# Kernel tuning notes

Hardware: AMD Instinct MI355X
Metric: run time of the kernel (lower is better)

Reference implementation:

```python
import jax, jax.numpy as jnp
import numpy as np

WINDOW = 1024  # sliding-window mask_mod: attend to keys within WINDOW behind the query


def setup_inputs() -> dict:
    key = jax.random.key(0)
    B, L, H, E = 2, 2048, 16, 64
    qkv = jax.random.normal(key, (B, L, 3, H, E), dtype=jnp.float32)
    return {"qkv": qkv}


def reference(qkv) -> jnp.ndarray:
    # Training path of FlexAttention.forward (key_cache/val_cache/cache_seqlens = None).
    B, L, _, H, E = qkv.shape
    q = qkv[:, :, 0]  # [b, l, h, e]
    k = qkv[:, :, 1]
    v = qkv[:, :, 2]

    scale = 1.0 / (E ** 0.5)  # flex_attention default softmax scaling
    scores = jnp.einsum("bqhe,bkhe->bhqk", q, k) * scale  # [b, h, q, kv]

    q_idx = jnp.arange(L)[:, None]
    kv_idx = jnp.arange(L)[None, :]
    dist = q_idx - kv_idx  # [q, kv]

    # score_mod: ALiBi bias, slope_h = 2^(-8*(h+1)/H)
    slopes = jnp.exp2(-8.0 * (jnp.arange(H, dtype=jnp.float32) + 1.0) / H)
    scores = scores - slopes[None, :, None, None] * dist.astype(jnp.float32)

    # and_masks(mask_mod, causal_mask): sliding window AND causal
    mask = (dist >= 0) & (dist < WINDOW)  # causal guarantees >=1 valid key per row
    scores = jnp.where(mask[None, None], scores, -jnp.inf)

    attn = jax.nn.softmax(scores, axis=-1)
    out = jnp.einsum("bhqk,bkhe->bqhe", attn, v)  # [b, l, h, e]
    return out
```

## Files before the change

kernel.cpp:

```cpp
#include <hip/hip_runtime.h>
#include <cstdint>

#define L_SEQ 2048
#define NH 16
#define EDIM 64
#define WINDOW 1024
#define QT 64
#define KT 64
#define LOG2E 1.4426950408889634f
#define M_FIX 16.0f

typedef short bf16x8 __attribute__((ext_vector_type(8)));
typedef short bf16x4 __attribute__((ext_vector_type(4)));
typedef float f32x4 __attribute__((ext_vector_type(4)));

__device__ __forceinline__ short f2bf(float x) {
    uint32_t u = __builtin_bit_cast(uint32_t, x);
    uint32_t r = (u + 0x7fffu + ((u >> 16) & 1u)) >> 16;
    return (short)(r & 0xffffu);
}
__device__ __forceinline__ short f2bf_trunc(float x) {
    return (short)(__builtin_bit_cast(uint32_t, x) >> 16);
}

__device__ __forceinline__ f32x4 mfma16(bf16x4 a, bf16x4 b, f32x4 c) {
#if __has_builtin(__builtin_amdgcn_mfma_f32_16x16x16bf16_1k)
    return __builtin_amdgcn_mfma_f32_16x16x16bf16_1k(a, b, c, 0, 0, 0);
#else
    asm("s_nop 1\n\tv_mfma_f32_16x16x16_bf16 %0, %1, %2, %0"
        : "+v"(c) : "v"(a), "v"(b));
    return c;
#endif
}

__device__ __forceinline__ void async16(const short* g, const short* l) {
    __builtin_amdgcn_global_load_lds(
        (const __attribute__((address_space(1))) void*)(uintptr_t)(g),
        (__attribute__((address_space(3))) void*)(uintptr_t)(l),
        16, 0, 0);
}

__global__ __launch_bounds__(256) void prepass4(const float* __restrict__ qkv,
        short* __restrict__ kw, short* __restrict__ vw) {
    __shared__ float vt[64][68];
    const int x = blockIdx.x;
    const int xcd = x & 7, y = x >> 3;
    const int pairid = xcd * 4 + (y >> 5);
    const int tile = y & 31;
    const int b = pairid >> 4, h = pairid & 15;
    const int tid = threadIdx.x;
    const int tg = pairid * 32 + tile;
    const float* base = qkv + (size_t)b * (L_SEQ * 3072) + (size_t)tile * 64 * 3072 + h * 64;
    short* ko = kw + (size_t)tg * 4096;
    short* vo = vw + (size_t)tg * 4096;

    #pragma unroll
    for (int it = 0; it < 2; ++it) {
        const int c = tid + it * 256;
        const int row = c >> 3, cc = (c & 7) ^ (row & 7);
        const float* src = base + (size_t)row * 3072 + 1024 + cc * 8;
        float4 a = *(const float4*)src, d = *(const float4*)(src + 4);
        short* o = ko + (size_t)c * 8;
        o[0] = f2bf(a.x); o[1] = f2bf(a.y); o[2] = f2bf(a.z); o[3] = f2bf(a.w);
        o[4] = f2bf(d.x); o[5] = f2bf(d.y); o[6] = f2bf(d.z); o[7] = f2bf(d.w);
    }
    {
        const int row = tid >> 2, e0 = (tid & 3) << 4;
        const float* src = base + (size_t)row * 3072 + 2048 + e0;
        #pragma unroll
        for (int q4 = 0; q4 < 4; ++q4) {
            float4 a = *(const float4*)(src + q4 * 4);
            vt[e0 + q4 * 4 + 0][row] = a.x;
            vt[e0 + q4 * 4 + 1][row] = a.y;
            vt[e0 + q4 * 4 + 2][row] = a.z;
            vt[e0 + q4 * 4 + 3][row] = a.w;
        }
    }
    __syncthreads();
    #pragma unroll
    for (int it = 0; it < 2; ++it) {
        const int c = tid + it * 256;
        const int et = c >> 7, a = (c >> 6) & 1, l6 = c & 63;
        const int quad = l6 >> 4, r16 = l6 & 15;
        const int e = et * 16 + r16;
        float4 x0 = *(const float4*)&vt[e][a * 32 + quad * 4];
        float4 x1 = *(const float4*)&vt[e][a * 32 + 16 + quad * 4];
        bf16x8 o8;
        o8[0] = f2bf(x0.x); o8[1] = f2bf(x0.y); o8[2] = f2bf(x0.z); o8[3] = f2bf(x0.w);
        o8[4] = f2bf(x1.x); o8[5] = f2bf(x1.y); o8[6] = f2bf(x1.z); o8[7] = f2bf(x1.w);
        *(bf16x8*)(vo + (size_t)c * 8) = o8;
    }
}

__global__ __launch_bounds__(256, 4) void flexattn_fwd7(
        const float* __restrict__ qkv, const short* __restrict__ kw,
        const short* __restrict__ vw, float* __restrict__ out) {
    __shared__ __align__(16) short kS[2][4096];
    __shared__ __align__(16) short vS[2][4096];

    const int s = blockIdx.y & 31;
    const int k = blockIdx.y >> 5;
    const int t16 = (s + ((k >> 1) << 4)) & 31;
    const int qtile = (k & 1) ? (31 - t16) : t16;
    const int pairid = blockIdx.x * 4 + k;
    const int h = pairid & 15;
    const int b = pairid >> 4;

    const int tid   = threadIdx.x;
    const int w     = tid >> 6;
    const int lane  = tid & 63;
    const int quad  = lane >> 4;
    const int r16   = lane & 15;
    const int qhalf = w & 1;
    const int khalf = w >> 1;
    const int qb    = qtile * QT;
    const int bh32  = (b * NH + h) * 32;
    const int q0    = qb + qhalf * 32 + r16;

    const int t0q = (qb >= WINDOW - 1) ? ((qb - (WINDOW - 1)) >> 6) : 0;
    const int t1  = qtile;
    const int swz = quad ^ (r16 & 7);
    const int cb0 = w * 128;

    {
        const short* ktile = kw + (size_t)(bh32 + t0q) * 4096;
        const short* vtile = vw + (size_t)(bh32 + t0q) * 4096;
        #pragma unroll
        for (int i = 0; i < 2; ++i) {
            const int cb = cb0 + i * 64;
            async16(ktile + (size_t)(cb + lane) * 8, &kS[0][cb * 8]);
            async16(vtile + (size_t)(cb + lane) * 8, &vS[0][cb * 8]);
        }
    }

    const float qscale = 0.125f * LOG2E;
    bf16x8 qfrag[2][2];
    #pragma unroll
    for (int g = 0; g < 2; ++g) {
        const float* qrow = qkv + (size_t)b * (L_SEQ * 3072)
                                + (size_t)(q0 + g * 16) * 3072 + h * 64;
        #pragma unroll
        for (int es = 0; es < 2; ++es) {
            const float* p = qrow + es * 32 + quad * 8;
            float4 a = *(const float4*)p;
            float4 c = *(const float4*)(p + 4);
            bf16x8 f;
            f[0] = f2bf(a.x * qscale); f[1] = f2bf(a.y * qscale);
            f[2] = f2bf(a.z * qscale); f[3] = f2bf(a.w * qscale);
            f[4] = f2bf(c.x * qscale); f[5] = f2bf(c.y * qscale);
            f[6] = f2bf(c.z * qscale); f[7] = f2bf(c.w * qscale);
            qfrag[g][es] = f;
        }
    }

    const float slope2 = __builtin_amdgcn_exp2f(-8.0f * (float)(h + 1) / (float)NH) * LOG2E;
    const float c64 = slope2 * 64.0f;
    f32x4 EA[2][2];
    #pragma unroll
    for (int g = 0; g < 2; ++g)
        #pragma unroll
        for (int ctl = 0; ctl < 2; ++ctl)
            #pragma unroll
            for (int r = 0; r < 4; ++r)
                EA[g][ctl][r] = slope2 * (float)(t0q * 64 + (khalf * 2 + ctl) * 16
                                                 + quad * 4 + r - (q0 + g * 16)) - M_FIX;

    f32x4 O[2][4] = {};
    float rs[2] = {0.f, 0.f};

    for (int kt = t0q; kt <= t1; ++kt) {
        const int cur = (kt - t0q) & 1;
        __syncthreads();
        if (kt < t1) {
            const int nb = cur ^ 1;
            const short* ktile = kw + (size_t)(bh32 + kt + 1) * 4096;
            const short* vtile = vw + (size_t)(bh32 + kt + 1) * 4096;
            #pragma unroll
            for (int i = 0; i < 2; ++i) {
                const int cb = cb0 + i * 64;
                async16(ktile + (size_t)(cb + lane) * 8, &kS[nb][cb * 8]);
                async16(vtile + (size_t)(cb + lane) * 8, &vS[nb][cb * 8]);
            }
        }

        f32x4 S[2][2];
        __builtin_amdgcn_s_setprio(1);
        #pragma unroll
        for (int ctl = 0; ctl < 2; ++ctl) {
            const int ct = khalf * 2 + ctl;
            const int c0 = ((ct * 16 + r16) << 3) + swz;
            bf16x8 k0 = *(const bf16x8*)&kS[cur][c0 * 8];
            bf16x8 k1 = *(const bf16x8*)&kS[cur][(c0 ^ 4) * 8];
            #pragma unroll
            for (int g = 0; g < 2; ++g) {
                f32x4 acc = __builtin_amdgcn_mfma_f32_16x16x32_bf16(k0, qfrag[g][0], EA[g][ctl], 0, 0, 0);
                S[g][ctl] = __builtin_amdgcn_mfma_f32_16x16x32_bf16(k1, qfrag[g][1], acc, 0, 0, 0);
            }
        }
        __builtin_amdgcn_s_setprio(0);

        bf16x4 pb[2][2];
        if (kt != t0q && kt != t1) {
            #pragma unroll
            for (int g = 0; g < 2; ++g)
                #pragma unroll
                for (int ctl = 0; ctl < 2; ++ctl)
                    #pragma unroll
                    for (int r = 0; r < 4; ++r) {
                        const float pe = __builtin_amdgcn_exp2f(S[g][ctl][r]);
                        rs[g] += pe;
                        pb[g][ctl][r] = f2bf_trunc(pe);
                    }
        } else {
            const int key0 = kt * 64 + khalf * 32 + quad * 4;
            #pragma unroll
            for (int g = 0; g < 2; ++g) {
                const int qg = q0 + g * 16;
                #pragma unroll
                for (int ctl = 0; ctl < 2; ++ctl)
                    #pragma unroll
                    for (int r = 0; r < 4; ++r) {
                        const int dist = qg - (key0 + ctl * 16 + r);
                        float pe = __builtin_amdgcn_exp2f(S[g][ctl][r]);
                        pe = (dist < 0 || dist >= WINDOW) ? 0.0f : pe;
                        rs[g] += pe;
                        pb[g][ctl][r] = f2bf_trunc(pe);
                    }
            }
        }

        __builtin_amdgcn_s_setprio(1);
        #pragma unroll
        for (int et = 0; et < 4; ++et) {
            bf16x8 v8 = *(const bf16x8*)&vS[cur][(size_t)((et * 2 + khalf) * 64 + lane) * 8];
            bf16x4 vlo = {v8[0], v8[1], v8[2], v8[3]};
            bf16x4 vhi = {v8[4], v8[5], v8[6], v8[7]};
            #pragma unroll
            for (int g = 0; g < 2; ++g) {
                O[g][et] = mfma16(vlo, pb[g][0], O[g][et]);
                O[g][et] = mfma16(vhi, pb[g][1], O[g][et]);
            }
        }
        __builtin_amdgcn_s_setprio(0);

        #pragma unroll
        for (int ctl = 0; ctl < 2; ++ctl) {
            EA[0][ctl] += c64;
            EA[1][ctl] += c64;
        }
    }

    __syncthreads();
    float* oS = (float*)&kS[0][0];
    float* rS = (float*)&vS[0][0];
    if (khalf) {
        float* dst = oS + qhalf * 2048;
        #pragma unroll
        for (int g = 0; g < 2; ++g)
            #pragma unroll
            for (int et = 0; et < 4; ++et)
                #pragma unroll
                for (int j = 0; j < 4; ++j)
                    dst[((g * 4 + et) * 4 + j) * 64 + lane] = O[g][et][j];
        rS[qhalf * 128 + lane]      = rs[0];
        rS[qhalf * 128 + 64 + lane] = rs[1];
    }
    __syncthreads();
    if (!khalf) {
        const float* src = oS + qhalf * 2048;
        #pragma unroll
        for (int g = 0; g < 2; ++g)
            #pragma unroll
            for (int et = 0; et < 4; ++et)
                #pragma unroll
                for (int j = 0; j < 4; ++j)
                    O[g][et][j] += src[((g * 4 + et) * 4 + j) * 64 + lane];
        rs[0] += rS[qhalf * 128 + lane];
        rs[1] += rS[qhalf * 128 + 64 + lane];

        #pragma unroll
        for (int g = 0; g < 2; ++g) {
            float r = rs[g];
            r += __shfl_xor(r, 16, 64);
            r += __shfl_xor(r, 32, 64);
            const float rl = 1.0f / r;
            float* op = out + ((size_t)b * L_SEQ + (q0 + g * 16)) * (NH * EDIM) + h * EDIM;
            #pragma unroll
            for (int et = 0; et < 4; ++et) {
                float4 o4 = {O[g][et][0] * rl, O[g][et][1] * rl,
                             O[g][et][2] * rl, O[g][et][3] * rl};
                *(float4*)(op + et * 16 + quad * 4) = o4;
            }
        }
    }
}

__global__ __launch_bounds__(256, 2) void flexattn_fwd_fb(
        const float* __restrict__ qkv, float* __restrict__ out) {
    __shared__ __align__(16) short kT[KT * 72];
    __shared__ __align__(16) short vB[8 * 64 * 8];
    __shared__ __align__(16) short pT[4][16 * 72];

    const int qtile = blockIdx.x;
    const int h     = blockIdx.y;
    const int b     = blockIdx.z;
    const int tid   = threadIdx.x;
    const int w     = tid >> 6;
    const int lane  = tid & 63;
    const int quad  = lane >> 4;
    const int r16   = lane & 15;
    const int qb = qtile * QT;
    const int rowstride = 3 * NH * EDIM;

    const float* qbase = qkv + ((size_t)b * L_SEQ * 3 + 0) * (NH * EDIM) + h * EDIM;
    const float* kbase = qkv + ((size_t)b * L_SEQ * 3 + 1) * (NH * EDIM) + h * EDIM;
    const float* vbase = qkv + ((size_t)b * L_SEQ * 3 + 2) * (NH * EDIM) + h * EDIM;

    const float qscale = 0.125f * LOG2E;
    bf16x8 qfrag[2];
    {
        const int qg = qb + w * 16 + r16;
        const float* qrow = qbase + (size_t)qg * rowstride;
        #pragma unroll
        for (int es = 0; es < 2; ++es) {
            const float* p = qrow + es * 32 + quad * 8;
            float4 a = *(const float4*)p;
            float4 c = *(const float4*)(p + 4);
            bf16x8 f;
            f[0] = f2bf(a.x * qscale); f[1] = f2bf(a.y * qscale);
            f[2] = f2bf(a.z * qscale); f[3] = f2bf(a.w * qscale);
            f[4] = f2bf(c.x * qscale); f[5] = f2bf(c.y * qscale);
            f[6] = f2bf(c.z * qscale); f[7] = f2bf(c.w * qscale);
            qfrag[es] = f;
        }
    }

    const float slope2 = __builtin_amdgcn_exp2f(-8.0f * (float)(h + 1) / (float)NH) * LOG2E;
    f32x4 O[4] = {{0,0,0,0},{0,0,0,0},{0,0,0,0},{0,0,0,0}};
    float m_run[4] = {-1e30f, -1e30f, -1e30f, -1e30f};
    float l_run[4] = {0.f, 0.f, 0.f, 0.f};

    const int kmin = (qb >= WINDOW - 1) ? (qb - (WINDOW - 1)) : 0;
    const int t0 = kmin >> 6;
    const int t1 = qtile;

    for (int kt = t0; kt <= t1; ++kt) {
        __syncthreads();
        {
            const int j = tid >> 2;
            const int ebase = (tid & 3) * 16;
            const float* krow = kbase + (size_t)(kt * KT + j) * rowstride + ebase;
            const float* vrow = vbase + (size_t)(kt * KT + j) * rowstride + ebase;
            const int js = j >> 5, qd = (j >> 3) & 3, ii = j & 7;
            #pragma unroll
            for (int ee = 0; ee < 4; ++ee) {
                const int e = ebase + ee * 4;
                float4 k4 = *(const float4*)(krow + ee * 4);
                short* kd = &kT[j * 72 + e];
                kd[0] = f2bf(k4.x); kd[1] = f2bf(k4.y);
                kd[2] = f2bf(k4.z); kd[3] = f2bf(k4.w);
                float4 v4 = *(const float4*)(vrow + ee * 4);
                const int et = e >> 4;
                const int ln = qd * 16 + (e & 15);
                short* vd = &vB[(((js * 4 + et) * 64) + ln) * 8 + ii];
                vd[0]  = f2bf(v4.x);
                vd[8]  = f2bf(v4.y);
                vd[16] = f2bf(v4.z);
                vd[24] = f2bf(v4.w);
            }
        }
        __syncthreads();

        f32x4 S[4];
        #pragma unroll
        for (int ct = 0; ct < 4; ++ct) {
            const short* kr = &kT[(ct * 16 + r16) * 72 + quad * 8];
            bf16x8 b0 = *(const bf16x8*)kr;
            bf16x8 b1 = *(const bf16x8*)(kr + 32);
            f32x4 acc = {0.f, 0.f, 0.f, 0.f};
            acc = __builtin_amdgcn_mfma_f32_16x16x32_bf16(qfrag[0], b0, acc, 0, 0, 0);
            acc = __builtin_amdgcn_mfma_f32_16x16x32_bf16(qfrag[1], b1, acc, 0, 0, 0);
            S[ct] = acc;
        }

        const int q0 = qb + w * 16 + quad * 4;
        float p[4][4];
        float mt[4] = {-1e30f, -1e30f, -1e30f, -1e30f};
        #pragma unroll
        for (int ct = 0; ct < 4; ++ct) {
            const int kg = kt * KT + ct * 16 + r16;
            #pragma unroll
            for (int r = 0; r < 4; ++r) {
                const int dist = q0 + r - kg;
                float s2 = S[ct][r] - slope2 * (float)dist;
                if (dist < 0 || dist >= WINDOW) s2 = -1e30f;
                p[ct][r] = s2;
                mt[r] = fmaxf(mt[r], s2);
            }
        }
        #pragma unroll
        for (int d = 1; d < 16; d <<= 1) {
            #pragma unroll
            for (int r = 0; r < 4; ++r)
                mt[r] = fmaxf(mt[r], __shfl_xor(mt[r], d, 64));
        }

        float alpha[4], rsum[4];
        #pragma unroll
        for (int r = 0; r < 4; ++r) {
            const float mn = fmaxf(m_run[r], mt[r]);
            alpha[r] = __builtin_amdgcn_exp2f(m_run[r] - mn);
            m_run[r] = mn;
            float sacc = 0.f;
            #pragma unroll
            for (int ct = 0; ct < 4; ++ct) {
                const float pe = __builtin_amdgcn_exp2f(p[ct][r] - mn);
                p[ct][r] = pe;
                sacc += pe;
            }
            rsum[r] = sacc;
        }
        #pragma unroll
        for (int d = 1; d < 16; d <<= 1) {
            #pragma unroll
            for (int r = 0; r < 4; ++r)
                rsum[r] += __shfl_xor(rsum[r], d, 64);
        }
        #pragma unroll
        for (int r = 0; r < 4; ++r)
            l_run[r] = l_run[r] * alpha[r] + rsum[r];
        #pragma unroll
        for (int et = 0; et < 4; ++et) {
            #pragma unroll
            for (int r = 0; r < 4; ++r)
                O[et][r] *= alpha[r];
        }

        short* pw = &pT[w][0];
        #pragma unroll
        for (int ct = 0; ct < 4; ++ct) {
            #pragma unroll
            for (int r = 0; r < 4; ++r)
                pw[(quad * 4 + r) * 72 + ct * 16 + r16] = f2bf(p[ct][r]);
        }
        bf16x8 aP0 = *(const bf16x8*)(pw + r16 * 72 + quad * 8);
        bf16x8 aP1 = *(const bf16x8*)(pw + r16 * 72 + 32 + quad * 8);

        #pragma unroll
        for (int et = 0; et < 4; ++et) {
            bf16x8 v0 = *(const bf16x8*)(&vB[((0 * 4 + et) * 64 + lane) * 8]);
            O[et] = __builtin_amdgcn_mfma_f32_16x16x32_bf16(aP0, v0, O[et], 0, 0, 0);
            bf16x8 v1 = *(const bf16x8*)(&vB[((1 * 4 + et) * 64 + lane) * 8]);
            O[et] = __builtin_amdgcn_mfma_f32_16x16x32_bf16(aP1, v1, O[et], 0, 0, 0);
        }
    }

    float* obase = out + (((size_t)b * L_SEQ) * NH + (size_t)h) * EDIM;
    #pragma unroll
    for (int r = 0; r < 4; ++r) {
        const int qg = qb + w * 16 + quad * 4 + r;
        const float rl = 1.0f / l_run[r];
        float* orow = obase + (size_t)qg * (NH * EDIM);
        #pragma unroll
        for (int et = 0; et < 4; ++et)
            orow[et * 16 + r16] = O[et][r] * rl;
    }
}

extern "C" void kernel_launch(void* const* d_in, const int* in_sizes, int n_in,
                              void* d_out, int out_size, void* d_ws, size_t ws_size,
                              hipStream_t stream) {
    const float* qkv = (const float*)d_in[0];
    float* out = (float*)d_out;
    const size_t need = (size_t)2 * 1024 * 4096 * sizeof(short);
    if (ws_size >= need) {
        short* kw = (short*)d_ws;
        short* vw = kw + (size_t)1024 * 4096;
        prepass4<<<1024, 256, 0, stream>>>(qkv, kw, vw);
        dim3 grid(8, 128);
        flexattn_fwd7<<<grid, 256, 0, stream>>>(qkv, kw, vw, out);
    } else {
        dim3 gridfb(L_SEQ / QT, NH, 2);
        flexattn_fwd_fb<<<gridfb, 256, 0, stream>>>(qkv, out);
    }
}
```

Baseline: 112.8 us.

## Triple-buffer K tiles and stagger K/V prefetch with partial vmcnt waits

The attention kernel now keeps three K tile buffers and two V buffers in LDS. It prefetches K two tiles ahead and V one tile ahead. The full __syncthreads is replaced by an explicit s_waitcnt vmcnt(4) plus barrier, placed before the QK stage and again before the PV stage, so the async loads still in flight do not stall the current tile. Q global loads are also issued before the first tile prefetch so their latency overlaps. The cost is more LDS per block, which may reduce occupancy, and the schedule depends on vmcnt counting being right, with redundant clamped loads at the tail.

```diff
diff --git a/kernel.cpp b/kernel.cpp
--- a/kernel.cpp
+++ b/kernel.cpp
@@ -39,6 +39,13 @@
         (__attribute__((address_space(3))) void*)(uintptr_t)(l),
         16, 0, 0);
 }
+
+#define SYNC_VMCNT4()                                           \
+    do {                                                        \
+        asm volatile("s_waitcnt vmcnt(4)" ::: "memory");        \
+        __builtin_amdgcn_s_barrier();                           \
+        __builtin_amdgcn_sched_barrier(0);                      \
+    } while (0)
 
 __global__ __launch_bounds__(256) void prepass4(const float* __restrict__ qkv,
         short* __restrict__ kw, short* __restrict__ vw) {
@@ -92,11 +99,11 @@
     }
 }
 
-__global__ __launch_bounds__(256, 4) void flexattn_fwd7(
+__global__ __launch_bounds__(256, 4) void flexattn_fwd8(
         const float* __restrict__ qkv, const short* __restrict__ kw,
         const short* __restrict__ vw, float* __restrict__ out) {
-    __shared__ __align__(16) short kS[2][4096];
-    __shared__ __align__(16) short vS[2][4096];
+    __shared__ __align__(16) short kB[3][4096];
+    __shared__ __align__(16) short vB2[2][4096];
 
     const int s = blockIdx.y & 31;
     const int k = blockIdx.y >> 5;
@@ -122,28 +129,43 @@
     const int swz = quad ^ (r16 & 7);
     const int cb0 = w * 128;
 
+    float4 qraw[2][2][2];
+    #pragma unroll
+    for (int g = 0; g < 2; ++g) {
+        const float* qrow = qkv + (size_t)b * (L_SEQ * 3072)
+                                + (size_t)(q0 + g * 16) * 3072 + h * 64;
+        #pragma unroll
+        for (int es = 0; es < 2; ++es) {
+            const float* p = qrow + es * 32 + quad * 8;
+            qraw[g][es][0] = *(const float4*)p;
+            qraw[g][es][1] = *(const float4*)(p + 4);
+        }
+    }
+
     {
-        const short* ktile = kw + (size_t)(bh32 + t0q) * 4096;
-        const short* vtile = vw + (size_t)(bh32 + t0q) * 4096;
-        #pragma unroll
-        for (int i = 0; i < 2; ++i) {
-            const int cb = cb0 + i * 64;
-            async16(ktile + (size_t)(cb + lane) * 8, &kS[0][cb * 8]);
-            async16(vtile + (size_t)(cb + lane) * 8, &vS[0][cb * 8]);
-        }
+        const int t0c1 = (t0q + 1 <= t1) ? t0q + 1 : t1;
+        const short* k0t = kw + (size_t)(bh32 + t0q) * 4096;
+        const short* k1t = kw + (size_t)(bh32 + t0c1) * 4096;
+        const short* v0t = vw + (size_t)(bh32 + t0q) * 4096;
+        short* kd0 = &kB[t0q % 3][0];
+        short* kd1 = &kB[(t0q + 1) % 3][0];
+        short* vd0 = &vB2[t0q & 1][0];
+        async16(k0t + (size_t)(cb0 + lane) * 8,      kd0 + (size_t)cb0 * 8);
+        async16(k0t + (size_t)(cb0 + 64 + lane) * 8, kd0 + (size_t)(cb0 + 64) * 8);
+        async16(k1t + (size_t)(cb0 + lane) * 8,      kd1 + (size_t)cb0 * 8);
+        async16(k1t + (size_t)(cb0 + 64 + lane) * 8, kd1 + (size_t)(cb0 + 64) * 8);
+        async16(v0t + (size_t)(cb0 + lane) * 8,      vd0 + (size_t)cb0 * 8);
+        async16(v0t + (size_t)(cb0 + 64 + lane) * 8, vd0 + (size_t)(cb0 + 64) * 8);
     }
 
     const float qscale = 0.125f * LOG2E;
     bf16x8 qfrag[2][2];
     #pragma unroll
     for (int g = 0; g < 2; ++g) {
-        const float* qrow = qkv + (size_t)b * (L_SEQ * 3072)
-                                + (size_t)(q0 + g * 16) * 3072 + h * 64;
         #pragma unroll
         for (int es = 0; es < 2; ++es) {
-            const float* p = qrow + es * 32 + quad * 8;
-            float4 a = *(const float4*)p;
-            float4 c = *(const float4*)(p + 4);
+            float4 a = qraw[g][es][0];
+            float4 c = qraw[g][es][1];
             bf16x8 f;
             f[0] = f2bf(a.x * qscale); f[1] = f2bf(a.y * qscale);
             f[2] = f2bf(a.z * qscale); f[3] = f2bf(a.w * qscale);
@@ -169,18 +191,22 @@
     float rs[2] = {0.f, 0.f};
 
     for (int kt = t0q; kt <= t1; ++kt) {
-        const int cur = (kt - t0q) & 1;
-        __syncthreads();
-        if (kt < t1) {
-            const int nb = cur ^ 1;
-            const short* ktile = kw + (size_t)(bh32 + kt + 1) * 4096;
-            const short* vtile = vw + (size_t)(bh32 + kt + 1) * 4096;
-            #pragma unroll
-            for (int i = 0; i < 2; ++i) {
-                const int cb = cb0 + i * 64;
-                async16(ktile + (size_t)(cb + lane) * 8, &kS[nb][cb * 8]);
-                async16(vtile + (size_t)(cb + lane) * 8, &vS[nb][cb * 8]);
-            }
+        const int kc = kt % 3;
+        const int vc = kt & 1;
+
+        SYNC_VMCNT4();
+
+        {
+            const int kpre = (kt + 2 <= t1) ? kt + 2 : t1;
+            const int vpre = (kt + 1 <= t1) ? kt + 1 : t1;
+            short* kd = &kB[(kt + 2) % 3][0];
+            short* vd = &vB2[(kt + 1) & 1][0];
+            const short* ktile = kw + (size_t)(bh32 + kpre) * 4096;
+            const short* vtile = vw + (size_t)(bh32 + vpre) * 4096;
+            async16(ktile + (size_t)(cb0 + lane) * 8,      kd + (size_t)cb0 * 8);
+            async16(ktile + (size_t)(cb0 + 64 + lane) * 8, kd + (size_t)(cb0 + 64) * 8);
+            async16(vtile + (size_t)(cb0 + lane) * 8,      vd + (size_t)cb0 * 8);
+            async16(vtile + (size_t)(cb0 + 64 + lane) * 8, vd + (size_t)(cb0 + 64) * 8);
         }
 
         f32x4 S[2][2];
@@ -189,8 +215,8 @@
         for (int ctl = 0; ctl < 2; ++ctl) {
             const int ct = khalf * 2 + ctl;
             const int c0 = ((ct * 16 + r16) << 3) + swz;
-            bf16x8 k0 = *(const bf16x8*)&kS[cur][c0 * 8];
-            bf16x8 k1 = *(const bf16x8*)&kS[cur][(c0 ^ 4) * 8];
+            bf16x8 k0 = *(const bf16x8*)&kB[kc][c0 * 8];
+            bf16x8 k1 = *(const bf16x8*)&kB[kc][(c0 ^ 4) * 8];
             #pragma unroll
             for (int g = 0; g < 2; ++g) {
                 f32x4 acc = __builtin_amdgcn_mfma_f32_16x16x32_bf16(k0, qfrag[g][0], EA[g][ctl], 0, 0, 0);
@@ -229,10 +255,12 @@
             }
         }
 
+        SYNC_VMCNT4();
+
         __builtin_amdgcn_s_setprio(1);
         #pragma unroll
         for (int et = 0; et < 4; ++et) {
-            bf16x8 v8 = *(const bf16x8*)&vS[cur][(size_t)((et * 2 + khalf) * 64 + lane) * 8];
+            bf16x8 v8 = *(const bf16x8*)&vB2[vc][(size_t)((et * 2 + khalf) * 64 + lane) * 8];
             bf16x4 vlo = {v8[0], v8[1], v8[2], v8[3]};
             bf16x4 vhi = {v8[4], v8[5], v8[6], v8[7]};
             #pragma unroll
@@ -251,8 +279,8 @@
     }
 
     __syncthreads();
-    float* oS = (float*)&kS[0][0];
-    float* rS = (float*)&vS[0][0];
+    float* oS = (float*)&kB[0][0];
+    float* rS = (float*)&vB2[0][0];
     if (khalf) {
         float* dst = oS + qhalf * 2048;
         #pragma unroll
@@ -478,7 +506,7 @@
         short* vw = kw + (size_t)1024 * 4096;
         prepass4<<<1024, 256, 0, stream>>>(qkv, kw, vw);
         dim3 grid(8, 128);
-        flexattn_fwd7<<<grid, 256, 0, stream>>>(qkv, kw, vw, out);
+        flexattn_fwd8<<<grid, 256, 0, stream>>>(qkv, kw, vw, out);
     } else {
         dim3 gridfb(L_SEQ / QT, NH, 2);
         flexattn_fwd_fb<<<gridfb, 256, 0, stream>>>(qkv, out);
```

New measurement: 113.4 us. No clear change (+0.5%).
